# Kernel tuning notes

Measured on AMD Instinct MI355X. Metric: run time of the kernel, lower is better.

The kernel has to match this reference:

```python
import jax, jax.numpy as jnp
import numpy as np


def setup_inputs() -> dict:
    key = jax.random.key(0)
    k1, k2, k3 = jax.random.split(key, 3)
    # N, C, H, W per input_specs
    x = jax.random.normal(k1, (16, 8, 1024, 1024), dtype=jnp.float32)
    # weight: (out_channels, in_channels, kH, kW)
    weight = jax.random.normal(k2, (8, 8, 3, 3), dtype=jnp.float32) * 0.1
    bias = jax.random.normal(k3, (8,), dtype=jnp.float32) * 0.1
    return {"x": x, "weight": weight, "bias": bias}


def reference(x, weight, bias):
    # DietConv2dV2's tiled per-kernel-column matmul loop is mathematically a
    # standard direct conv2d (stride=1, padding=1) followed by a bias add.
    out = jax.lax.conv_general_dilated(
        x, weight,
        window_strides=(1, 1),
        padding=((1, 1), (1, 1)),
        dimension_numbers=("NCHW", "OIHW", "NCHW"),
    )
    return out + bias[None, :, None, None]
```

## Files before the change

### kernel.cpp

```cpp
#include <hip/hip_runtime.h>


#define R 4
#define HH 1024
#define WW 1024
#define CI 8
#define CO 8

__global__ __launch_bounds__(256) void conv3x3_kernel(
    const float* __restrict__ x,
    const float* __restrict__ wgt,
    const float* __restrict__ bias,
    float* __restrict__ out)
{
    const int w  = blockIdx.x * 256 + threadIdx.x;
    const int h0 = blockIdx.y * R;
    const int n  = blockIdx.z;

    const long HW = (long)HH * WW;
    const float* xn = x + (long)n * CI * HW;

    float acc[CO][R];
#pragma unroll
    for (int co = 0; co < CO; ++co) {
        const float b = bias[co];
#pragma unroll
        for (int r = 0; r < R; ++r) acc[co][r] = b;
    }

    for (int ci = 0; ci < CI; ++ci) {
        const float* xc = xn + (long)ci * HW;

        float in[R + 2][3];
#pragma unroll
        for (int r = 0; r < R + 2; ++r) {
            const int h = h0 - 1 + r;
            const bool hv = (h >= 0) && (h < HH);
            const float* row = xc + (long)h * WW;
#pragma unroll
            for (int c = 0; c < 3; ++c) {
                const int wc = w - 1 + c;
                const bool v = hv && (wc >= 0) && (wc < WW);
                in[r][c] = v ? row[wc] : 0.0f;
            }
        }

#pragma unroll
        for (int co = 0; co < CO; ++co) {
            const float* wp = wgt + ((co * CI + ci) * 9);
            float wv[9];
#pragma unroll
            for (int k = 0; k < 9; ++k) wv[k] = wp[k];
#pragma unroll
            for (int r = 0; r < R; ++r) {
#pragma unroll
                for (int kh = 0; kh < 3; ++kh) {
#pragma unroll
                    for (int kw = 0; kw < 3; ++kw) {
                        acc[co][r] = fmaf(in[r + kh][kw], wv[kh * 3 + kw], acc[co][r]);
                    }
                }
            }
        }
    }

#pragma unroll
    for (int co = 0; co < CO; ++co) {
        float* op = out + ((long)n * CO + co) * HW + (long)h0 * WW + w;
#pragma unroll
        for (int r = 0; r < R; ++r) {
            op[(long)r * WW] = acc[co][r];
        }
    }
}

extern "C" void kernel_launch(void* const* d_in, const int* in_sizes, int n_in,
                              void* d_out, int out_size, void* d_ws, size_t ws_size,
                              hipStream_t stream) {
    const float* x    = (const float*)d_in[0];
    const float* wgt  = (const float*)d_in[1];
    const float* bias = (const float*)d_in[2];
    float* out = (float*)d_out;

    dim3 grid(WW / 256, HH / R, 16);
    dim3 block(256, 1, 1);
    conv3x3_kernel<<<grid, block, 0, stream>>>(x, wgt, bias, out);
}
```

Baseline: 322.5 us.

## Rewrite 3x3 conv as bf16 MFMA implicit GEMM with LDS tiles

Replaces the scalar FMA direct convolution with an implicit GEMM on MFMA 16x16x32 bf16 instructions. Each block stages a 10-row by 132-column tile in LDS, with the 8 input channels converted to bf16 and packed into int4, and computes 8 output rows by 124 columns. Other changes: a 1D grid with XCD-aware block remapping, overlapping last column tile, and float4 stores. Converting inputs and weights to bf16 lowers precision versus the fp32 reference, and the column tiles overlap, so some halo loads are repeated.

```diff
diff --git a/kernel.cpp b/kernel.cpp
--- a/kernel.cpp
+++ b/kernel.cpp
@@ -1,75 +1,148 @@
 #include <hip/hip_runtime.h>
 
 
-#define R 4
+typedef __attribute__((ext_vector_type(8))) short short8;
+typedef __attribute__((ext_vector_type(4))) float f32x4;
+
 #define HH 1024
 #define WW 1024
-#define CI 8
-#define CO 8
+#define HW (1024*1024)
+#define WB 124
+#define HB 8
+#define SROWS 10
+#define UROW 132
+#define GX 9
+#define GY 128
+#define GZ 16
+#define NBLK (GX*GY*GZ)
 
-__global__ __launch_bounds__(256) void conv3x3_kernel(
+__device__ __forceinline__ unsigned short f2bf(float f) {
+    unsigned u = __float_as_uint(f);
+    return (unsigned short)((u + 0x7FFFu + ((u >> 16) & 1u)) >> 16);
+}
+
+__global__ __launch_bounds__(256) void conv3x3_mfma(
     const float* __restrict__ x,
     const float* __restrict__ wgt,
     const float* __restrict__ bias,
     float* __restrict__ out)
 {
-    const int w  = blockIdx.x * 256 + threadIdx.x;
-    const int h0 = blockIdx.y * R;
-    const int n  = blockIdx.z;
+    __shared__ int4 lds[SROWS * UROW];
 
-    const long HW = (long)HH * WW;
-    const float* xn = x + (long)n * CI * HW;
+    const int tid  = threadIdx.x;
+    const int lane = tid & 63;
+    const int wv   = tid >> 6;
+    const int l15  = lane & 15;
+    const int ch   = lane >> 4;
 
-    float acc[CO][R];
+    const unsigned bid  = blockIdx.x;
+    const unsigned work = (bid & 7u) * (NBLK / 8u) + (bid >> 3);
+    const int wz = (int)(work / (GX * GY));
+    const unsigned r1 = work - (unsigned)wz * (GX * GY);
+    const int wy = (int)(r1 / GX);
+    const int wx = (int)(r1 - (unsigned)wy * GX);
+
+    const int h0 = wy * HB;
+    const int w0 = (wx == GX - 1) ? (WW - WB) : wx * WB;
+
+    const float* xn = x + (size_t)wz * 8 * HW;
+
+    const int t0  = ch;
+    const int kh0 = (t0 >= 3) ? 1 : 0;
+    const int kw0 = t0 - 3 * kh0;
+    const int t1  = 4 + ch;
+    const int kh1 = (t1 >= 6) ? 2 : 1;
+    const int kw1 = t1 - 3 * kh1;
+    const int off0 = kh0 * UROW + kw0;
+    const int off1 = kh1 * UROW + kw1;
+    const int off2 = 2 * UROW + 2;
+
+    const int  coc = (l15 < 8) ? l15 : 7;
+    const bool com = (l15 < 8);
+    short8 b0, b1, b2;
+    {
+        const float* wp0 = wgt + coc * 72 + kh0 * 3 + kw0;
+        const float* wp1 = wgt + coc * 72 + kh1 * 3 + kw1;
+        const float* wp2 = wgt + coc * 72 + 2 * 3 + 2;
 #pragma unroll
-    for (int co = 0; co < CO; ++co) {
-        const float b = bias[co];
+        for (int j = 0; j < 8; ++j) {
+            b0[j] = (short)(com ? f2bf(wp0[j * 9]) : 0);
+            b1[j] = (short)(com ? f2bf(wp1[j * 9]) : 0);
+            b2[j] = (short)((com && ch == 0) ? f2bf(wp2[j * 9]) : 0);
+        }
+    }
+    const float bv = com ? bias[l15] : 0.0f;
+
+    for (int row = wv; row < SROWS; row += 4) {
+        const int gh = h0 - 1 + row;
+        if ((unsigned)gh < (unsigned)HH) {
 #pragma unroll
-        for (int r = 0; r < R; ++r) acc[co][r] = b;
+            for (int half = 0; half < 2; ++half) {
+                const int wl = lane + 64 * half;
+                const int gw = w0 - 1 + wl;
+                const bool wok = ((unsigned)gw < (unsigned)WW);
+                const int gwc = wok ? gw : 0;
+                const size_t boff = (size_t)gh * WW + gwc;
+                float v[8];
+#pragma unroll
+                for (int ci = 0; ci < 8; ++ci) {
+                    float t = xn[(size_t)ci * HW + boff];
+                    v[ci] = wok ? t : 0.0f;
+                }
+                int4 pk;
+                pk.x = (int)f2bf(v[0]) | ((int)f2bf(v[1]) << 16);
+                pk.y = (int)f2bf(v[2]) | ((int)f2bf(v[3]) << 16);
+                pk.z = (int)f2bf(v[4]) | ((int)f2bf(v[5]) << 16);
+                pk.w = (int)f2bf(v[6]) | ((int)f2bf(v[7]) << 16);
+                lds[row * UROW + wl] = pk;
+            }
+        } else {
+            int4 z; z.x = z.y = z.z = z.w = 0;
+            lds[row * UROW + lane]      = z;
+            lds[row * UROW + lane + 64] = z;
+        }
     }
+    __syncthreads();
 
-    for (int ci = 0; ci < CI; ++ci) {
-        const float* xc = xn + (long)ci * HW;
-
-        float in[R + 2][3];
+    f32x4 acc[2][8];
 #pragma unroll
-        for (int r = 0; r < R + 2; ++r) {
-            const int h = h0 - 1 + r;
-            const bool hv = (h >= 0) && (h < HH);
-            const float* row = xc + (long)h * WW;
+    for (int th = 0; th < 2; ++th)
 #pragma unroll
-            for (int c = 0; c < 3; ++c) {
-                const int wc = w - 1 + c;
-                const bool v = hv && (wc >= 0) && (wc < WW);
-                in[r][c] = v ? row[wc] : 0.0f;
-            }
+        for (int wt = 0; wt < 8; ++wt) {
+            acc[th][wt].x = bv; acc[th][wt].y = bv;
+            acc[th][wt].z = bv; acc[th][wt].w = bv;
         }
 
 #pragma unroll
-        for (int co = 0; co < CO; ++co) {
-            const float* wp = wgt + ((co * CI + ci) * 9);
-            float wv[9];
+    for (int th = 0; th < 2; ++th) {
+        const int hl = wv * 2 + th;
+        const int ub = hl * UROW + l15;
 #pragma unroll
-            for (int k = 0; k < 9; ++k) wv[k] = wp[k];
-#pragma unroll
-            for (int r = 0; r < R; ++r) {
-#pragma unroll
-                for (int kh = 0; kh < 3; ++kh) {
-#pragma unroll
-                    for (int kw = 0; kw < 3; ++kw) {
-                        acc[co][r] = fmaf(in[r + kh][kw], wv[kh * 3 + kw], acc[co][r]);
-                    }
-                }
-            }
+        for (int wt = 0; wt < 8; ++wt) {
+            const int u = ub + wt * 16;
+            short8 a0 = *reinterpret_cast<const short8*>(&lds[u + off0]);
+            short8 a1 = *reinterpret_cast<const short8*>(&lds[u + off1]);
+            short8 a2 = *reinterpret_cast<const short8*>(&lds[u + off2]);
+            f32x4 c = acc[th][wt];
+            c = __builtin_amdgcn_mfma_f32_16x16x32_bf16(a0, b0, c, 0, 0, 0);
+            c = __builtin_amdgcn_mfma_f32_16x16x32_bf16(a1, b1, c, 0, 0, 0);
+            c = __builtin_amdgcn_mfma_f32_16x16x32_bf16(a2, b2, c, 0, 0, 0);
+            acc[th][wt] = c;
         }
     }
 
+    if (com) {
 #pragma unroll
-    for (int co = 0; co < CO; ++co) {
-        float* op = out + ((long)n * CO + co) * HW + (long)h0 * WW + w;
+        for (int th = 0; th < 2; ++th) {
+            const int hl = wv * 2 + th;
+            float* op = out + ((size_t)wz * 8 + l15) * HW
+                            + (size_t)(h0 + hl) * WW + w0;
 #pragma unroll
-        for (int r = 0; r < R; ++r) {
-            op[(long)r * WW] = acc[co][r];
+            for (int wt = 0; wt < 8; ++wt) {
+                if (wt == 7 && ch == 3) continue;
+                *reinterpret_cast<float4*>(op + wt * 16 + ch * 4) =
+                    *reinterpret_cast<const float4*>(&acc[th][wt]);
+            }
         }
     }
 }
@@ -82,7 +155,7 @@
     const float* bias = (const float*)d_in[2];
     float* out = (float*)d_out;
 
-    dim3 grid(WW / 256, HH / R, 16);
+    dim3 grid(NBLK, 1, 1);
     dim3 block(256, 1, 1);
-    conv3x3_kernel<<<grid, block, 0, stream>>>(x, wgt, bias, out);
+    conv3x3_mfma<<<grid, block, 0, stream>>>(x, wgt, bias, out);
 }
```

Result: no change. 325.1 us (+0.8%).
